# Kernel optimization log

Measured on AMD Instinct MI355X. Metric: run time of the kernel, lower is better.

Reference implementation:

```python
import jax, jax.numpy as jnp
import numpy as np
from jax import lax

IMG = 800.0
PRE_NMS = 2000
POST_NMS = 1000
IOU_T = 0.7
BBOX_XFORM_CLIP = float(np.log(1000.0 / 16.0))


def build_anchors():
    # torchvision FPN anchor generator: one size per level, 3 aspect ratios
    strides = [4, 8, 16, 32, 64]
    sizes = [32, 64, 128, 256, 512]
    ratios = [0.5, 1.0, 2.0]
    out = []
    for s, sz in zip(strides, sizes):
        f = int(np.ceil(800 / s))  # feature map side
        base = []
        for r in ratios:
            w = sz * np.sqrt(1.0 / r)
            h = sz * np.sqrt(r)
            base.append([-w / 2, -h / 2, w / 2, h / 2])
        base = np.asarray(base)  # [3,4]
        sx = (np.arange(f) + 0.5) * s
        sy = (np.arange(f) + 0.5) * s
        yy, xx = np.meshgrid(sy, sx, indexing='ij')
        shifts = np.stack([xx, yy, xx, yy], -1).reshape(-1, 1, 4)
        out.append((shifts + base).reshape(-1, 4))
    return np.concatenate(out, 0).astype(np.float32)  # [159882,4]


def setup_inputs() -> dict:
    key = jax.random.key(0)
    k1, k2 = jax.random.split(key)
    B = 16
    anchors = jnp.asarray(build_anchors())
    A = anchors.shape[0]
    scores = jax.random.normal(k1, (B, A), dtype=jnp.float32)
    deltas = jax.random.normal(k2, (B, A, 4), dtype=jnp.float32) * 0.1
    return {"scores": scores, "deltas": deltas, "anchors": anchors}


def decode_boxes(deltas, anchors):
    wa = anchors[:, 2] - anchors[:, 0]
    ha = anchors[:, 3] - anchors[:, 1]
    cxa = anchors[:, 0] + 0.5 * wa
    cya = anchors[:, 1] + 0.5 * ha
    dx, dy = deltas[:, 0], deltas[:, 1]
    dw = jnp.minimum(deltas[:, 2], BBOX_XFORM_CLIP)
    dh = jnp.minimum(deltas[:, 3], BBOX_XFORM_CLIP)
    cx = dx * wa + cxa
    cy = dy * ha + cya
    w = jnp.exp(dw) * wa
    h = jnp.exp(dh) * ha
    boxes = jnp.stack([cx - 0.5 * w, cy - 0.5 * h, cx + 0.5 * w, cy + 0.5 * h], -1)
    return jnp.clip(boxes, 0.0, IMG)


def box_iou(a, b):
    # a: [N,4], b: [M,4]
    area_a = (a[:, 2] - a[:, 0]) * (a[:, 3] - a[:, 1])
    area_b = (b[:, 2] - b[:, 0]) * (b[:, 3] - b[:, 1])
    lt = jnp.maximum(a[:, None, :2], b[None, :, :2])
    rb = jnp.minimum(a[:, None, 2:], b[None, :, 2:])
    wh = jnp.clip(rb - lt, 0.0)
    inter = wh[..., 0] * wh[..., 1]
    return inter / (area_a[:, None] + area_b[None, :] - inter + 1e-9)


def greedy_nms_keep(boxes, iou_t):
    # boxes are sorted by descending score
    K = boxes.shape[0]
    iou = box_iou(boxes, boxes)  # [K,K]
    idx = jnp.arange(K)

    def body(i, keep):
        sup = (iou[i] > iou_t) & keep[i] & (idx > i)
        return keep & ~sup

    return lax.fori_loop(0, K, body, jnp.ones((K,), bool))


def _process_image(scores_i, deltas_i, anchors):
    # top-k pre-NMS on objectness logits (torchvision RPN order)
    top_logits, idx = lax.top_k(scores_i, PRE_NMS)
    boxes = decode_boxes(deltas_i[idx], anchors[idx])  # [PRE,4]
    keep = greedy_nms_keep(boxes, IOU_T)
    masked = jnp.where(keep, top_logits, -jnp.inf)
    kept_logits, idx2 = lax.top_k(masked, POST_NMS)
    kept_boxes = boxes[idx2]
    valid = jnp.isfinite(kept_logits)
    probs = jax.nn.sigmoid(jnp.where(valid, kept_logits, 0.0))
    out_boxes = jnp.where(valid[:, None], kept_boxes, 0.0)
    out_scores = jnp.where(valid, probs, 0.0)
    return jnp.concatenate([out_boxes, out_scores[:, None]], -1)  # [POST,5]


def reference(scores, deltas, anchors):
    return jax.vmap(_process_image, in_axes=(0, 0, None))(scores, deltas, anchors)
```

## Files before the change

### kernel.cpp

```cpp
#include <hip/hip_runtime.h>
#include <math.h>

#define PRE_NMS 2000
#define POST_NMS 1000
#define IOU_T 0.7f
#define IMGSZ 800.0f
#define CAP 6144
#define SORTN 2048
#define NBINS 1024
#define NWORDS 32
#define NSLICE 16
#define MROWS 2048
#define NTILES 528
#define TCAP 104

typedef unsigned long long u64;

__device__ __forceinline__ unsigned key_of(float f) {
    unsigned u = __float_as_uint(f);
    return (u & 0x80000000u) ? ~u : (u | 0x80000000u);
}
__device__ __forceinline__ float inv_key(unsigned k) {
    unsigned u = (k & 0x80000000u) ? (k ^ 0x80000000u) : ~k;
    return __uint_as_float(u);
}

__global__ __launch_bounds__(256) void hist_kernel(
    const float* __restrict__ scores, int A, unsigned* __restrict__ ghist,
    int* __restrict__ cand_cnt) {
  int b = blockIdx.x, slice = blockIdx.y;
  __shared__ unsigned h[NBINS];
  int tid = threadIdx.x;
  for (int i = tid; i < NBINS; i += 256) h[i] = 0;
  if (slice == 0 && tid == 0) cand_cnt[b] = 0;
  __syncthreads();
  int per = (A + NSLICE - 1) / NSLICE;
  int lo = slice * per, hi = min(lo + per, A);
  const float* sc = scores + (size_t)b * A;
  for (int i = lo + tid; i < hi; i += 256)
    atomicAdd(&h[key_of(sc[i]) >> 22], 1u);
  __syncthreads();
  unsigned* gh = ghist + ((size_t)b * NSLICE + slice) * NBINS;
  for (int i = tid; i < NBINS; i += 256) gh[i] = h[i];
}

__global__ __launch_bounds__(256) void compact_kernel(
    const float* __restrict__ scores, int A, const unsigned* __restrict__ ghist,
    u64* __restrict__ cand, int* __restrict__ cand_cnt, int* __restrict__ T1) {
  int b = blockIdx.x, slice = blockIdx.y;
  int tid = threadIdx.x;
  int lane = tid & 63, wave = tid >> 6;
  __shared__ unsigned sa[2][NBINS];
  __shared__ int sT;
  for (int i = tid; i < NBINS; i += 256) {
    unsigned s = 0;
    const unsigned* gh = ghist + (size_t)b * NSLICE * NBINS + i;
    #pragma unroll
    for (int s16 = 0; s16 < NSLICE; ++s16) s += gh[s16 * NBINS];
    sa[0][i] = s;
  }
  __syncthreads();
  int src = 0;
  for (int d = 1; d < NBINS; d <<= 1) {
    for (int i = tid; i < NBINS; i += 256)
      sa[src ^ 1][i] = sa[src][i] + ((i + d < NBINS) ? sa[src][i + d] : 0u);
    __syncthreads();
    src ^= 1;
  }
  for (int i = tid; i < NBINS; i += 256) {
    unsigned v = sa[src][i];
    unsigned nx = (i < NBINS - 1) ? sa[src][i + 1] : 0u;
    if (v >= PRE_NMS && nx < PRE_NMS) sT = i;
  }
  __syncthreads();
  int T = sT;
  if (slice == 0 && tid == 0) T1[b] = T;
  int per = (A + NSLICE - 1) / NSLICE;
  int lo = slice * per, hi = min(lo + per, A);
  const float* sc = scores + (size_t)b * A;
  int cnt = 0;
  for (int i = lo + tid; i < hi; i += 256)
    cnt += ((int)(key_of(sc[i]) >> 22) >= T);
  int pfx = cnt;
  #pragma unroll
  for (int d = 1; d < 64; d <<= 1) {
    int t2 = __shfl_up(pfx, d, 64);
    if (lane >= d) pfx += t2;
  }
  __shared__ int s_wt[4];
  __shared__ int s_base;
  if (lane == 63) s_wt[wave] = pfx;
  __syncthreads();
  if (tid == 0) {
    int tot = s_wt[0] + s_wt[1] + s_wt[2] + s_wt[3];
    int acc = 0;
    #pragma unroll
    for (int w2 = 0; w2 < 4; ++w2) { int t3 = s_wt[w2]; s_wt[w2] = acc; acc += t3; }
    s_base = atomicAdd(&cand_cnt[b], tot);
  }
  __syncthreads();
  int my_off = s_base + s_wt[wave] + (pfx - cnt);
  u64* cb = cand + (size_t)b * CAP;
  for (int i = lo + tid; i < hi; i += 256) {
    unsigned k = key_of(sc[i]);
    if ((int)(k >> 22) >= T) {
      if (my_off < CAP) cb[my_off] = ((u64)k << 32) | (unsigned)(~i);
      my_off++;
    }
  }
}

__global__ __launch_bounds__(1024) void refine_select_kernel(
    const u64* __restrict__ cand, const int* __restrict__ cand_cnt,
    const int* __restrict__ T1,
    u64* __restrict__ gsel, int* __restrict__ sel_cnt) {
  int b = blockIdx.x, tid = threadIdx.x;
  int lane = tid & 63;
  __shared__ unsigned h2[NBINS];
  __shared__ unsigned tmp[NBINS];
  __shared__ int s_above, s_sel, s_T2;
  int n = min(cand_cnt[b], CAP);
  const u64* cb = cand + (size_t)b * CAP;
  h2[tid] = 0;
  if (tid == 0) { s_above = 0; s_sel = 0; }
  __syncthreads();
  int T1v = T1[b];
  int loc = 0;
  for (int i = tid; i < n; i += 1024) {
    unsigned k = (unsigned)(cb[i] >> 32);
    if ((int)(k >> 22) > T1v) loc++;
    else atomicAdd(&h2[(k >> 12) & 1023], 1u);
  }
  for (int d = 32; d; d >>= 1) loc += __shfl_down(loc, d, 64);
  if (lane == 0 && loc) atomicAdd(&s_above, loc);
  __syncthreads();
  unsigned v = h2[tid];
  for (int d = 1; d < NBINS; d <<= 1) {
    tmp[tid] = v;
    __syncthreads();
    if (tid + d < NBINS) v += tmp[tid + d];
    __syncthreads();
  }
  tmp[tid] = v;
  __syncthreads();
  int above = s_above;
  unsigned nextv = (tid < NBINS - 1) ? tmp[tid + 1] : 0u;
  if (above + (int)v >= PRE_NMS && above + (int)nextv < PRE_NMS) s_T2 = tid;
  __syncthreads();
  unsigned thresh20 = ((unsigned)T1v << 10) | (unsigned)s_T2;
  u64* gs = gsel + (size_t)b * SORTN;
  for (int i = tid; i < n; i += 1024) {
    u64 cv = cb[i];
    if ((unsigned)(cv >> 44) >= thresh20) {
      int pos = atomicAdd(&s_sel, 1);
      if (pos < SORTN) gs[pos] = cv;
    }
  }
  __syncthreads();
  if (tid == 0) sel_cnt[b] = min(s_sel, SORTN);
}

__global__ __launch_bounds__(256) void rank_decode_kernel(
    const u64* __restrict__ gsel, const int* __restrict__ sel_cnt,
    const float* __restrict__ deltas, const float* __restrict__ anchors, int A,
    float* __restrict__ boxes, float* __restrict__ topk_logit) {
  int b = blockIdx.x, ci = blockIdx.y;
  int tid = threadIdx.x;
  __shared__ u64 keys[SORTN];
  __shared__ int s_part[256];
  const u64* gs = gsel + (size_t)b * SORTN;
  int n = sel_cnt[b];
  for (int i = tid; i < SORTN; i += 256)
    keys[i] = (i < n) ? gs[i] : 0ULL;
  __syncthreads();
  int half = tid >> 7;
  int li = tid & 127;
  int i = ci * 128 + li;
  u64 my = keys[i];
  int rank = 0;
  const ulonglong2* k2 = (const ulonglong2*)(keys + half * (SORTN / 2));
  #pragma unroll 4
  for (int j = 0; j < SORTN / 4; ++j) {
    ulonglong2 kk = k2[j];
    rank += (kk.x > my) + (kk.y > my);
  }
  s_part[tid] = rank;
  __syncthreads();
  if (half == 0) {
    rank = s_part[tid] + s_part[tid + 128];
    if (i < n && rank < PRE_NMS) {
      int a = (int)(~(unsigned)my);
      topk_logit[b * PRE_NMS + rank] = inv_key((unsigned)(my >> 32));
      const float CLIP = 4.135166556742356f;
      float4 dl = ((const float4*)deltas)[(size_t)b * A + a];
      float4 an = ((const float4*)anchors)[a];
      float wa = __fsub_rn(an.z, an.x);
      float ha = __fsub_rn(an.w, an.y);
      float cxa = __fadd_rn(an.x, __fmul_rn(0.5f, wa));
      float cya = __fadd_rn(an.y, __fmul_rn(0.5f, ha));
      float dw = fminf(dl.z, CLIP), dh = fminf(dl.w, CLIP);
      float cx = __fadd_rn(__fmul_rn(dl.x, wa), cxa);
      float cy = __fadd_rn(__fmul_rn(dl.y, ha), cya);
      float w2 = __fmul_rn((float)exp((double)dw), wa);
      float h2f = __fmul_rn((float)exp((double)dh), ha);
      float x1 = __fsub_rn(cx, __fmul_rn(0.5f, w2));
      float y1 = __fsub_rn(cy, __fmul_rn(0.5f, h2f));
      float x2 = __fadd_rn(cx, __fmul_rn(0.5f, w2));
      float y2 = __fadd_rn(cy, __fmul_rn(0.5f, h2f));
      x1 = fminf(fmaxf(x1, 0.f), IMGSZ);
      y1 = fminf(fmaxf(y1, 0.f), IMGSZ);
      x2 = fminf(fmaxf(x2, 0.f), IMGSZ);
      y2 = fminf(fmaxf(y2, 0.f), IMGSZ);
      ((float4*)boxes)[(size_t)b * PRE_NMS + rank] = make_float4(x1, y1, x2, y2);
    }
  }
}

__global__ __launch_bounds__(64) void iou_tile(
    const float* __restrict__ boxes, u64* __restrict__ maskT,
    unsigned* __restrict__ tflag) {
  int k = blockIdx.x;
  int b = blockIdx.y;
  int wj = (int)((sqrtf(8.0f * k + 1.0f) - 1.0f) * 0.5f);
  while ((wj + 1) * (wj + 2) / 2 <= k) ++wj;
  while (wj * (wj + 1) / 2 > k) --wj;
  int ti = k - wj * (wj + 1) / 2;
  int lane = threadIdx.x;
  int i = ti * 64 + lane;
  const float4* bb = (const float4*)boxes + (size_t)b * PRE_NMS;
  __shared__ float4 sbox[64];
  int jg = wj * 64 + lane;
  sbox[lane] = bb[min(jg, PRE_NMS - 1)];
  float4 A4 = bb[min(i, PRE_NMS - 1)];
  __syncthreads();
  float area_a = __fmul_rn(__fsub_rn(A4.z, A4.x), __fsub_rn(A4.w, A4.y));
  u64 m = 0;
  #pragma unroll 8
  for (int jj = 0; jj < 64; ++jj) {
    float4 Bb = sbox[jj];
    float area_b = __fmul_rn(__fsub_rn(Bb.z, Bb.x), __fsub_rn(Bb.w, Bb.y));
    float ltx = fmaxf(A4.x, Bb.x), lty = fmaxf(A4.y, Bb.y);
    float rbx = fminf(A4.z, Bb.z), rby = fminf(A4.w, Bb.w);
    float iw = fmaxf(__fsub_rn(rbx, ltx), 0.f);
    float ih = fmaxf(__fsub_rn(rby, lty), 0.f);
    float inter = __fmul_rn(iw, ih);
    float denom = __fadd_rn(__fsub_rn(__fadd_rn(area_a, area_b), inter), 1e-9f);
    int j = wj * 64 + jj;
    if (j > i && inter > __fmul_rn(IOU_T, denom)) m |= 1ULL << jj;
  }
  u64 anyb = __ballot(m != 0ULL);
  if (anyb) maskT[((size_t)b * NWORDS + wj) * MROWS + i] = m;
  if (lane == 0) tflag[(size_t)b * NTILES + k] = (anyb != 0ULL) ? 1u : 0u;
}

__global__ __launch_bounds__(256, 1) void nms_scan(
    const u64* __restrict__ maskT, const unsigned* __restrict__ tflag,
    const float* __restrict__ boxes,
    const float* __restrict__ logits, float* __restrict__ out) {
  int b = blockIdx.x;
  int tid = threadIdx.x;
  int lane = tid & 63, wave = tid >> 6;
  __shared__ u64 tiles[TCAP][64];
  __shared__ unsigned wflags[NWORDS];
  __shared__ int wbase[NWORDS];
  __shared__ unsigned short slot2cw[TCAP];
  __shared__ int s_nact;
  __shared__ u64 s_keep[NWORDS];
  __shared__ int pre[NWORDS];
  __shared__ int s_tot;
  const unsigned* tf = tflag + (size_t)b * NTILES;
  const u64* mb = maskT + (size_t)b * NWORDS * MROWS;
  if (tid < NWORDS) {
    int c = tid;
    unsigned wf = 0;
    for (int w2 = c; w2 < NWORDS; ++w2)
      if (tf[w2 * (w2 + 1) / 2 + c]) wf |= 1u << w2;
    wflags[c] = wf;
  }
  __syncthreads();
  if (tid == 0) {
    int s = 0;
    for (int c = 0; c < NWORDS; ++c) {
      wbase[c] = s;
      unsigned wf = wflags[c];
      while (wf) {
        int w2 = __ffs(wf) - 1; wf &= wf - 1;
        if (s < TCAP) slot2cw[s] = (unsigned short)((w2 << 8) | c);
        s++;
      }
    }
    s_nact = s;
  }
  __syncthreads();
  int nstage = min(s_nact, TCAP);
  for (int g = tid; g < nstage * 64; g += 256) {
    int slot = g >> 6, r = g & 63;
    unsigned cw = slot2cw[slot];
    int c = cw & 0xFF, w2 = cw >> 8;
    tiles[slot][r] = mb[(size_t)w2 * MROWS + c * 64 + r];
  }
  __syncthreads();
  if (wave == 0) {
    u64 keep = (lane < NWORDS) ? ((lane == NWORDS - 1) ? 0xFFFFULL : ~0ULL) : 0ULL;
    for (int c = 0; c < NWORDS; ++c) {
      unsigned wf = wflags[c];
      int base = wbase[c];
      u64 cur = __shfl(keep, c, 64);
      if ((wf >> c) & 1u) {
        int slot = base;
        u64 d = (slot < TCAP) ? tiles[slot][lane]
                              : mb[(size_t)c * MROWS + c * 64 + lane];
        unsigned dlo = (unsigned)d, dhi = (unsigned)(d >> 32);
        unsigned clo = __builtin_amdgcn_readfirstlane((unsigned)cur);
        unsigned chi = __builtin_amdgcn_readfirstlane((unsigned)(cur >> 32));
        #pragma unroll
        for (int bb = 0; bb < 32; ++bb) {
          unsigned rlo = __builtin_amdgcn_readlane(dlo, bb);
          unsigned rhi = __builtin_amdgcn_readlane(dhi, bb);
          unsigned msk = 0u - ((clo >> bb) & 1u);
          clo &= ~(rlo & msk);
          chi &= ~(rhi & msk);
        }
        #pragma unroll
        for (int bb = 0; bb < 32; ++bb) {
          unsigned rlo = __builtin_amdgcn_readlane(dlo, bb + 32);
          unsigned rhi = __builtin_amdgcn_readlane(dhi, bb + 32);
          unsigned msk = 0u - ((chi >> bb) & 1u);
          clo &= ~(rlo & msk);
          chi &= ~(rhi & msk);
        }
        cur = ((u64)chi << 32) | clo;
        keep = (lane == c) ? cur : keep;
      }
      unsigned rem = wf & ~((2u << c) - 1u);
      while (rem) {
        int w2 = __ffs(rem) - 1; rem &= rem - 1;
        int slot = base + __popc(wf & ((1u << w2) - 1u));
        u64 row = (slot < TCAP) ? tiles[slot][lane]
                                : mb[(size_t)w2 * MROWS + c * 64 + lane];
        u64 bit = (cur >> lane) & 1ULL;
        u64 v = row & (0ULL - bit);
        v |= __shfl_xor(v, 1, 64);
        v |= __shfl_xor(v, 2, 64);
        v |= __shfl_xor(v, 4, 64);
        v |= __shfl_xor(v, 8, 64);
        v |= __shfl_xor(v, 16, 64);
        v |= __shfl_xor(v, 32, 64);
        keep = (lane == w2) ? (keep & ~v) : keep;
      }
    }
    if (lane < NWORDS) s_keep[lane] = keep;
  }
  __syncthreads();
  if (tid == 0) {
    int acc = 0;
    for (int ww = 0; ww < NWORDS; ++ww) {
      pre[ww] = acc;
      acc += __popcll(s_keep[ww]);
    }
    s_tot = acc;
  }
  __syncthreads();
  const float* lg_b = logits + b * PRE_NMS;
  const float4* bx_b = (const float4*)boxes + (size_t)b * PRE_NMS;
  for (int i = tid; i < PRE_NMS; i += 256) {
    u64 wv = s_keep[i >> 6];
    if ((wv >> (i & 63)) & 1) {
      int rank = pre[i >> 6] + __popcll(wv & ((1ULL << (i & 63)) - 1ULL));
      if (rank < POST_NMS) {
        float4 bx = bx_b[i];
        float lg = lg_b[i];
        float e = (float)exp(-(double)lg);
        float pp = 1.0f / (1.0f + e);
        float* o = out + ((size_t)b * POST_NMS + rank) * 5;
        o[0] = bx.x; o[1] = bx.y; o[2] = bx.z; o[3] = bx.w; o[4] = pp;
      }
    }
  }
  int tot = s_tot;
  for (int j = tid; j < POST_NMS; j += 256) {
    if (j >= tot) {
      float* o = out + ((size_t)b * POST_NMS + j) * 5;
      o[0] = 0.f; o[1] = 0.f; o[2] = 0.f; o[3] = 0.f; o[4] = 0.f;
    }
  }
}

extern "C" void kernel_launch(void* const* d_in, const int* in_sizes, int n_in,
                              void* d_out, int out_size, void* d_ws, size_t ws_size,
                              hipStream_t stream) {
  const float* scores  = (const float*)d_in[0];
  const float* deltas  = (const float*)d_in[1];
  const float* anchors = (const float*)d_in[2];
  int A = in_sizes[2] / 4;
  int B = in_sizes[0] / A;

  char* ws = (char*)d_ws;
  size_t off = 0;
  auto alloc = [&](size_t bytes) {
    void* p = ws + off;
    off += (bytes + 255) & ~(size_t)255;
    return p;
  };
  unsigned* ghist    = (unsigned*)alloc((size_t)B * NSLICE * NBINS * 4);
  int*      cand_cnt = (int*)alloc((size_t)B * 4);
  int*      T1       = (int*)alloc((size_t)B * 4);
  u64*      cand     = (u64*)alloc((size_t)B * CAP * 8);
  u64*      gsel     = (u64*)alloc((size_t)B * SORTN * 8);
  int*      sel_cnt  = (int*)alloc((size_t)B * 4);
  float*    topk_lg  = (float*)alloc((size_t)B * PRE_NMS * 4);
  float*    boxes    = (float*)alloc((size_t)B * PRE_NMS * 16);
  u64*      maskT    = (u64*)alloc((size_t)B * NWORDS * MROWS * 8);
  unsigned* tflag    = (unsigned*)alloc((size_t)B * NTILES * 4);

  hist_kernel<<<dim3(B, NSLICE), 256, 0, stream>>>(scores, A, ghist, cand_cnt);
  compact_kernel<<<dim3(B, NSLICE), 256, 0, stream>>>(scores, A, ghist, cand, cand_cnt, T1);
  refine_select_kernel<<<B, 1024, 0, stream>>>(cand, cand_cnt, T1, gsel, sel_cnt);
  rank_decode_kernel<<<dim3(B, SORTN / 128), 256, 0, stream>>>(
      gsel, sel_cnt, deltas, anchors, A, boxes, topk_lg);
  iou_tile<<<dim3(NTILES, B), 64, 0, stream>>>(boxes, maskT, tflag);
  nms_scan<<<B, 256, 0, stream>>>(maskT, tflag, boxes, topk_lg, (float*)d_out);
}
```

Measured before the change: 205.7 us.

## Use atomic word-flag bitmasks and sparse lane scans in NMS scan

The iou_tile kernel now builds per-column word flag bitmasks with atomicOr instead of writing a flag per tile, so nms_scan no longer reads and assembles the triangular tile flag array. The scan loop visits only columns that have nonzero flags, found through a ballot. The six-step shuffle OR reduction is replaced by a ballot followed by readlane over only the lanes whose value is nonzero. This cuts serial latency in the single-wave scan when suppression is sparse, at the cost of global atomics and a data-dependent loop that could grow when many lanes are active.

```diff
diff --git a/kernel.cpp b/kernel.cpp
--- a/kernel.cpp
+++ b/kernel.cpp
@@ -27,12 +27,15 @@
 
 __global__ __launch_bounds__(256) void hist_kernel(
     const float* __restrict__ scores, int A, unsigned* __restrict__ ghist,
-    int* __restrict__ cand_cnt) {
+    int* __restrict__ cand_cnt, unsigned* __restrict__ gwf) {
   int b = blockIdx.x, slice = blockIdx.y;
   __shared__ unsigned h[NBINS];
   int tid = threadIdx.x;
   for (int i = tid; i < NBINS; i += 256) h[i] = 0;
-  if (slice == 0 && tid == 0) cand_cnt[b] = 0;
+  if (slice == 0) {
+    if (tid == 0) cand_cnt[b] = 0;
+    if (tid < NWORDS) gwf[b * NWORDS + tid] = 0u;
+  }
   __syncthreads();
   int per = (A + NSLICE - 1) / NSLICE;
   int lo = slice * per, hi = min(lo + per, A);
@@ -218,7 +221,7 @@
 
 __global__ __launch_bounds__(64) void iou_tile(
     const float* __restrict__ boxes, u64* __restrict__ maskT,
-    unsigned* __restrict__ tflag) {
+    unsigned* __restrict__ gwf) {
   int k = blockIdx.x;
   int b = blockIdx.y;
   int wj = (int)((sqrtf(8.0f * k + 1.0f) - 1.0f) * 0.5f);
@@ -249,40 +252,35 @@
     if (j > i && inter > __fmul_rn(IOU_T, denom)) m |= 1ULL << jj;
   }
   u64 anyb = __ballot(m != 0ULL);
-  if (anyb) maskT[((size_t)b * NWORDS + wj) * MROWS + i] = m;
-  if (lane == 0) tflag[(size_t)b * NTILES + k] = (anyb != 0ULL) ? 1u : 0u;
+  if (anyb) {
+    maskT[((size_t)b * NWORDS + wj) * MROWS + i] = m;
+    if (lane == 0) atomicOr(&gwf[b * NWORDS + ti], 1u << wj);
+  }
 }
 
 __global__ __launch_bounds__(256, 1) void nms_scan(
-    const u64* __restrict__ maskT, const unsigned* __restrict__ tflag,
+    const u64* __restrict__ maskT, const unsigned* __restrict__ gwf,
     const float* __restrict__ boxes,
     const float* __restrict__ logits, float* __restrict__ out) {
   int b = blockIdx.x;
   int tid = threadIdx.x;
   int lane = tid & 63, wave = tid >> 6;
   __shared__ u64 tiles[TCAP][64];
-  __shared__ unsigned wflags[NWORDS];
+  __shared__ unsigned swf[NWORDS];
   __shared__ int wbase[NWORDS];
   __shared__ unsigned short slot2cw[TCAP];
   __shared__ int s_nact;
   __shared__ u64 s_keep[NWORDS];
   __shared__ int pre[NWORDS];
   __shared__ int s_tot;
-  const unsigned* tf = tflag + (size_t)b * NTILES;
   const u64* mb = maskT + (size_t)b * NWORDS * MROWS;
-  if (tid < NWORDS) {
-    int c = tid;
-    unsigned wf = 0;
-    for (int w2 = c; w2 < NWORDS; ++w2)
-      if (tf[w2 * (w2 + 1) / 2 + c]) wf |= 1u << w2;
-    wflags[c] = wf;
-  }
+  if (tid < NWORDS) swf[tid] = gwf[b * NWORDS + tid];
   __syncthreads();
   if (tid == 0) {
     int s = 0;
     for (int c = 0; c < NWORDS; ++c) {
       wbase[c] = s;
-      unsigned wf = wflags[c];
+      unsigned wf = swf[c];
       while (wf) {
         int w2 = __ffs(wf) - 1; wf &= wf - 1;
         if (s < TCAP) slot2cw[s] = (unsigned short)((w2 << 8) | c);
@@ -302,9 +300,13 @@
   __syncthreads();
   if (wave == 0) {
     u64 keep = (lane < NWORDS) ? ((lane == NWORDS - 1) ? 0xFFFFULL : ~0ULL) : 0ULL;
-    for (int c = 0; c < NWORDS; ++c) {
-      unsigned wf = wflags[c];
-      int base = wbase[c];
+    unsigned wfreg = (lane < NWORDS) ? swf[lane] : 0u;
+    int baser = (lane < NWORDS) ? wbase[lane] : 0;
+    unsigned wmask = (unsigned)__ballot(wfreg != 0u);
+    while (wmask) {
+      int c = __ffs(wmask) - 1; wmask &= wmask - 1;
+      unsigned wf = __shfl(wfreg, c, 64);
+      int base = __shfl(baser, c, 64);
       u64 cur = __shfl(keep, c, 64);
       if ((wf >> c) & 1u) {
         int slot = base;
@@ -332,7 +334,7 @@
         cur = ((u64)chi << 32) | clo;
         keep = (lane == c) ? cur : keep;
       }
-      unsigned rem = wf & ~((2u << c) - 1u);
+      unsigned rem = wf & ~(1u << c);
       while (rem) {
         int w2 = __ffs(rem) - 1; rem &= rem - 1;
         int slot = base + __popc(wf & ((1u << w2) - 1u));
@@ -340,13 +342,15 @@
                                 : mb[(size_t)w2 * MROWS + c * 64 + lane];
         u64 bit = (cur >> lane) & 1ULL;
         u64 v = row & (0ULL - bit);
-        v |= __shfl_xor(v, 1, 64);
-        v |= __shfl_xor(v, 2, 64);
-        v |= __shfl_xor(v, 4, 64);
-        v |= __shfl_xor(v, 8, 64);
-        v |= __shfl_xor(v, 16, 64);
-        v |= __shfl_xor(v, 32, 64);
-        keep = (lane == w2) ? (keep & ~v) : keep;
+        u64 mnz = __ballot(v != 0ULL);
+        u64 sv = 0;
+        while (mnz) {
+          int l = (int)__ffsll((long long)mnz) - 1; mnz &= mnz - 1;
+          unsigned slo = __builtin_amdgcn_readlane((unsigned)v, l);
+          unsigned shi = __builtin_amdgcn_readlane((unsigned)(v >> 32), l);
+          sv |= ((u64)shi << 32) | slo;
+        }
+        keep = (lane == w2) ? (keep & ~sv) : keep;
       }
     }
     if (lane < NWORDS) s_keep[lane] = keep;
@@ -411,13 +415,13 @@
   float*    topk_lg  = (float*)alloc((size_t)B * PRE_NMS * 4);
   float*    boxes    = (float*)alloc((size_t)B * PRE_NMS * 16);
   u64*      maskT    = (u64*)alloc((size_t)B * NWORDS * MROWS * 8);
-  unsigned* tflag    = (unsigned*)alloc((size_t)B * NTILES * 4);
-
-  hist_kernel<<<dim3(B, NSLICE), 256, 0, stream>>>(scores, A, ghist, cand_cnt);
+  unsigned* gwf      = (unsigned*)alloc((size_t)B * NWORDS * 4);
+
+  hist_kernel<<<dim3(B, NSLICE), 256, 0, stream>>>(scores, A, ghist, cand_cnt, gwf);
   compact_kernel<<<dim3(B, NSLICE), 256, 0, stream>>>(scores, A, ghist, cand, cand_cnt, T1);
   refine_select_kernel<<<B, 1024, 0, stream>>>(cand, cand_cnt, T1, gsel, sel_cnt);
   rank_decode_kernel<<<dim3(B, SORTN / 128), 256, 0, stream>>>(
       gsel, sel_cnt, deltas, anchors, A, boxes, topk_lg);
-  iou_tile<<<dim3(NTILES, B), 64, 0, stream>>>(boxes, maskT, tflag);
-  nms_scan<<<B, 256, 0, stream>>>(maskT, tflag, boxes, topk_lg, (float*)d_out);
-}
+  iou_tile<<<dim3(NTILES, B), 64, 0, stream>>>(boxes, maskT, gwf);
+  nms_scan<<<B, 256, 0, stream>>>(maskT, gwf, boxes, topk_lg, (float*)d_out);
+}
```

New measurement: 196.2 us, median of 2. 1.05x faster.
